# Kernel tuning notes

Hardware: AMD Instinct MI355X
Metric: run time of the kernel (lower is better)

## Reference

```python
import jax, jax.numpy as jnp
import numpy as np

N_ENS = 10   # LSTMs per ensemble
N_OPP = 5    # opponents
H_GEN = 10   # gen LSTM hidden
H_OPP = 5    # opp LSTM hidden


def setup_inputs() -> dict:
    key = jax.random.key(0)
    ks = iter(jax.random.split(key, 32))
    r = lambda shape, s=0.1: jax.random.normal(next(ks), shape, dtype=jnp.float32) * s
    return {
        "x": jax.random.normal(next(ks), (1, 1, 37), dtype=jnp.float32),
        # 10 gen LSTMs (input 12, hidden 10), stacked; torch gate order i,f,g,o
        "W_ih_gen": r((N_ENS, 4 * H_GEN, 12)),
        "W_hh_gen": r((N_ENS, 4 * H_GEN, H_GEN)),
        "b_ih_gen": r((N_ENS, 4 * H_GEN)),
        "b_hh_gen": r((N_ENS, 4 * H_GEN)),
        "h0_gen": r((N_ENS, H_GEN)),
        "c0_gen": r((N_ENS, H_GEN)),
        # 10 opp-game LSTMs (input 4, hidden 5), shared weights across opponents
        "W_ih_game": r((N_ENS, 4 * H_OPP, 4)),
        "W_hh_game": r((N_ENS, 4 * H_OPP, H_OPP)),
        "b_ih_game": r((N_ENS, 4 * H_OPP)),
        "b_hh_game": r((N_ENS, 4 * H_OPP)),
        # per-opponent, per-ensemble-member hidden/cell states
        "h0_game": r((N_OPP, N_ENS, H_OPP)),
        "c0_game": r((N_OPP, N_ENS, H_OPP)),
        # decision MLP
        "W1": r((50, 200)), "b1": r((50,)),
        "W2": r((10, 50)), "b2": r((10,)),
        "W3": r((1, 10)), "b3": r((1,)),
    }


def reference(x, W_ih_gen, W_hh_gen, b_ih_gen, b_hh_gen, h0_gen, c0_gen,
              W_ih_game, W_hh_game, b_ih_game, b_hh_game, h0_game, c0_game,
              W1, b1, W2, b2, W3, b3):
    xv = x[0, 0]  # seq_len = batch = 1 is forced by the 200-feature reshape

    # --- gen ensemble: 10 independent LSTM cells batched as one GEMM ---
    x_gen = xv[:12]
    g = (jnp.einsum('khi,i->kh', W_ih_gen, x_gen)
         + jnp.einsum('khj,kj->kh', W_hh_gen, h0_gen)
         + b_ih_gen + b_hh_gen)                      # [10, 40]
    ig, fg, gg, og = jnp.split(g, 4, axis=-1)
    c_gen = jax.nn.sigmoid(fg) * c0_gen + jax.nn.sigmoid(ig) * jnp.tanh(gg)
    h_gen = jax.nn.sigmoid(og) * jnp.tanh(c_gen)      # [10, 10]
    x_gen_out = h_gen.reshape(-1)                     # [100]

    # --- opponent game ensembles: 5 opps x 10 LSTMs batched ---
    x_opp = xv[12:].reshape(N_OPP, 5)
    active = x_opp[:, 0]
    xin = x_opp[:, 1:]                                # [5, 4]
    g2 = (jnp.einsum('khi,oi->okh', W_ih_game, xin)
          + jnp.einsum('khj,okj->okh', W_hh_game, h0_game)
          + b_ih_game + b_hh_game)                    # [5, 10, 20]
    i2, f2, g2g, o2 = jnp.split(g2, 4, axis=-1)
    c_game = jax.nn.sigmoid(f2) * c0_game + jax.nn.sigmoid(i2) * jnp.tanh(g2g)
    h_game = jax.nn.sigmoid(o2) * jnp.tanh(c_game)    # [5, 10, 5]

    # Source bug preserved: the 'round' loop concatenates x_opp_game (output of
    # the LAST game LSTM, i=9) ten more times; round-LSTM outputs never reach
    # the model output, so they are omitted here.
    feat = jnp.concatenate(
        [h_game.reshape(N_OPP, -1),                     # 10*5 = 50
         jnp.tile(h_game[:, -1, :], (1, N_ENS))],       # 10*5 = 50 (repeated)
        axis=1)                                         # [5, 100]

    # if int(x_active) == 1 -> truncation toward zero then equality with 1
    mask = (jnp.trunc(active) == 1).astype(feat.dtype)  # [5]
    cnt = mask.sum()
    avg = jnp.where(cnt > 0,
                    (mask[:, None] * feat).sum(0) / jnp.maximum(cnt, 1.0),
                    jnp.zeros((100,), feat.dtype))       # [100]

    h1 = jnp.tanh(jnp.concatenate([x_gen_out, avg]) @ W1.T + b1)
    h2 = jnp.tanh(h1 @ W2.T + b2)
    out = jnp.tanh(h2 @ W3.T + b3)
    return out.reshape(1, 1, 1)
```

## Files before the change

### kernel.cpp

```cpp
#include <hip/hip_runtime.h>

__device__ __forceinline__ float sigf(float x) { return 1.0f / (1.0f + expf(-x)); }

__global__ __launch_bounds__(512) void net6max_kernel(
    const float* __restrict__ x,
    const float* __restrict__ W_ih_gen, const float* __restrict__ W_hh_gen,
    const float* __restrict__ b_ih_gen, const float* __restrict__ b_hh_gen,
    const float* __restrict__ h0_gen,  const float* __restrict__ c0_gen,
    const float* __restrict__ W_ih_game, const float* __restrict__ W_hh_game,
    const float* __restrict__ b_ih_game, const float* __restrict__ b_hh_game,
    const float* __restrict__ h0_game, const float* __restrict__ c0_game,
    const float* __restrict__ W1, const float* __restrict__ b1,
    const float* __restrict__ W2, const float* __restrict__ b2,
    const float* __restrict__ W3, const float* __restrict__ b3,
    float* __restrict__ out)
{
    __shared__ float xs[37];
    __shared__ float g_gen[400];
    __shared__ float g2[1000];
    __shared__ float hg[100];
    __shared__ float hgame[250];
    __shared__ float in200[200];
    __shared__ float h1v[50];
    __shared__ float h2v[10];

    const int tid = threadIdx.x;

    if (tid < 37) xs[tid] = x[tid];
    __syncthreads();

    if (tid < 400) {
        const int k = tid / 40, h = tid % 40;
        float s = b_ih_gen[tid] + b_hh_gen[tid];
        const float* wi = W_ih_gen + (k * 40 + h) * 12;
        #pragma unroll
        for (int i = 0; i < 12; ++i) s += wi[i] * xs[i];
        const float* wh = W_hh_gen + (k * 40 + h) * 10;
        const float* h0 = h0_gen + k * 10;
        #pragma unroll
        for (int j = 0; j < 10; ++j) s += wh[j] * h0[j];
        g_gen[tid] = s;
    }
    for (int e = tid; e < 1000; e += 512) {
        const int o = e / 200, rem = e % 200;
        const int k = rem / 20, h = rem % 20;
        float s = b_ih_game[k * 20 + h] + b_hh_game[k * 20 + h];
        const float* wi = W_ih_game + (k * 20 + h) * 4;
        const float* xi = xs + 12 + o * 5 + 1;
        #pragma unroll
        for (int i = 0; i < 4; ++i) s += wi[i] * xi[i];
        const float* wh = W_hh_game + (k * 20 + h) * 5;
        const float* h0 = h0_game + (o * 10 + k) * 5;
        #pragma unroll
        for (int j = 0; j < 5; ++j) s += wh[j] * h0[j];
        g2[e] = s;
    }
    __syncthreads();

    if (tid < 100) {
        const int k = tid / 10, j = tid % 10;
        const float ig = g_gen[k*40 +      j];
        const float fg = g_gen[k*40 + 10 + j];
        const float gg = g_gen[k*40 + 20 + j];
        const float og = g_gen[k*40 + 30 + j];
        const float c  = sigf(fg) * c0_gen[tid] + sigf(ig) * tanhf(gg);
        hg[tid] = sigf(og) * tanhf(c);
    }
    if (tid >= 256 && tid < 506) {
        const int e = tid - 256;
        const int o = e / 50, rem = e % 50, k = rem / 5, j = rem % 5;
        const int base = (o * 10 + k) * 20;
        const float ig = g2[base +      j];
        const float fg = g2[base +  5 + j];
        const float gg = g2[base + 10 + j];
        const float og = g2[base + 15 + j];
        const float c  = sigf(fg) * c0_game[e] + sigf(ig) * tanhf(gg);
        hgame[e] = sigf(og) * tanhf(c);
    }
    __syncthreads();

    if (tid < 100) in200[tid] = hg[tid];
    if (tid >= 128 && tid < 228) {
        const int c = tid - 128;
        float cnt = 0.f, s = 0.f;
        #pragma unroll
        for (int o = 0; o < 5; ++o) {
            const float m = (truncf(xs[12 + o * 5]) == 1.0f) ? 1.0f : 0.0f;
            cnt += m;
            const float f = (c < 50) ? hgame[o * 50 + c]
                                     : hgame[o * 50 + 45 + (c - 50) % 5];
            s += m * f;
        }
        in200[100 + c] = (cnt > 0.f) ? (s / cnt) : 0.f;
    }
    __syncthreads();

    if (tid < 200) {
        const int row = tid >> 2, seg = tid & 3;
        const float* w = W1 + row * 200 + seg * 50;
        const float* v = in200 + seg * 50;
        float p = 0.f;
        #pragma unroll
        for (int c = 0; c < 50; ++c) p += w[c] * v[c];
        p += __shfl_down(p, 2);
        p += __shfl_down(p, 1);
        if (seg == 0) h1v[row] = tanhf(p + b1[row]);
    }
    __syncthreads();

    if (tid < 10) {
        const float* w = W2 + tid * 50;
        float s = b2[tid];
        #pragma unroll
        for (int c = 0; c < 50; ++c) s += w[c] * h1v[c];
        h2v[tid] = tanhf(s);
    }
    __syncthreads();

    if (tid == 0) {
        float s = b3[0];
        #pragma unroll
        for (int c = 0; c < 10; ++c) s += W3[c] * h2v[c];
        out[0] = tanhf(s);
    }
}

extern "C" void kernel_launch(void* const* d_in, const int* in_sizes, int n_in,
                              void* d_out, int out_size, void* d_ws, size_t ws_size,
                              hipStream_t stream) {
    (void)in_sizes; (void)n_in; (void)out_size; (void)d_ws; (void)ws_size;
    net6max_kernel<<<1, 512, 0, stream>>>(
        (const float*)d_in[0],
        (const float*)d_in[1],
        (const float*)d_in[2],
        (const float*)d_in[3],
        (const float*)d_in[4],
        (const float*)d_in[5],
        (const float*)d_in[6],
        (const float*)d_in[7],
        (const float*)d_in[8],
        (const float*)d_in[9],
        (const float*)d_in[10],
        (const float*)d_in[11],
        (const float*)d_in[12],
        (const float*)d_in[13],
        (const float*)d_in[14],
        (const float*)d_in[15],
        (const float*)d_in[16],
        (const float*)d_in[17],
        (const float*)d_in[18],
        (float*)d_out);
}
```

Baseline: 11.63 us.

## Prefetch MLP weights into registers and fuse LSTM gate phases to cut barriers

Each thread now computes all four gates of its LSTM unit and applies the cell update directly, which removes the gate-preactivation shared buffers and one barrier. The W1/W2/W3 weights and biases are loaded into registers at kernel start so their global latency overlaps the LSTM phase. The layer-2 and layer-3 stages are merged into one wavefront using a shuffle reduction, removing another barrier. The block also shrinks to 384 threads. The cost is more registers per thread (two 50-float arrays), which risks spilling, and less parallelism in the gate computation.

Measured after the change: 12.19 us. 4.8% more time.

```diff
diff --git a/kernel.cpp b/kernel.cpp
--- a/kernel.cpp
+++ b/kernel.cpp
@@ -2,7 +2,7 @@
 
 __device__ __forceinline__ float sigf(float x) { return 1.0f / (1.0f + expf(-x)); }
 
-__global__ __launch_bounds__(512) void net6max_kernel(
+__global__ __launch_bounds__(384) void net6max_kernel(
     const float* __restrict__ x,
     const float* __restrict__ W_ih_gen, const float* __restrict__ W_hh_gen,
     const float* __restrict__ b_ih_gen, const float* __restrict__ b_hh_gen,
@@ -15,113 +15,115 @@
     const float* __restrict__ W3, const float* __restrict__ b3,
     float* __restrict__ out)
 {
-    __shared__ float xs[37];
-    __shared__ float g_gen[400];
-    __shared__ float g2[1000];
     __shared__ float hg[100];
     __shared__ float hgame[250];
-    __shared__ float in200[200];
-    __shared__ float h1v[50];
-    __shared__ float h2v[10];
+    __shared__ float avg_s[100];
+    __shared__ float h1v[52];
 
     const int tid = threadIdx.x;
 
-    if (tid < 37) xs[tid] = x[tid];
-    __syncthreads();
+    float w1r[50];
+    float b1r = 0.f;
+    if (tid < 200) {
+        const int row = tid >> 2, seg = tid & 3;
+        const float* w = W1 + row * 200 + seg * 50;
+        #pragma unroll
+        for (int c = 0; c < 50; ++c) w1r[c] = w[c];
+        if (seg == 0) b1r = b1[row];
+    }
+    float w2r[50];
+    float b2r = 0.f, w3r = 0.f, b3r = 0.f;
+    if (tid < 10) {
+        const float* w = W2 + tid * 50;
+        #pragma unroll
+        for (int c = 0; c < 50; ++c) w2r[c] = w[c];
+        b2r = b2[tid];
+        w3r = W3[tid];
+    }
+    if (tid == 0) b3r = b3[0];
 
-    if (tid < 400) {
-        const int k = tid / 40, h = tid % 40;
-        float s = b_ih_gen[tid] + b_hh_gen[tid];
-        const float* wi = W_ih_gen + (k * 40 + h) * 12;
+    if (tid < 100) {
+        const int k = tid / 10, j = tid % 10;
+        float acc[4];
         #pragma unroll
-        for (int i = 0; i < 12; ++i) s += wi[i] * xs[i];
-        const float* wh = W_hh_gen + (k * 40 + h) * 10;
-        const float* h0 = h0_gen + k * 10;
+        for (int g = 0; g < 4; ++g) {
+            const int r = k * 40 + g * 10 + j;
+            float s = b_ih_gen[r] + b_hh_gen[r];
+            const float* wi = W_ih_gen + r * 12;
+            #pragma unroll
+            for (int i = 0; i < 12; ++i) s += wi[i] * x[i];
+            const float* wh = W_hh_gen + r * 10;
+            const float* h0 = h0_gen + k * 10;
+            #pragma unroll
+            for (int jj = 0; jj < 10; ++jj) s += wh[jj] * h0[jj];
+            acc[g] = s;
+        }
+        const float c = sigf(acc[1]) * c0_gen[tid] + sigf(acc[0]) * tanhf(acc[2]);
+        hg[tid] = sigf(acc[3]) * tanhf(c);
+    }
+    if (tid >= 128 && tid < 378) {
+        const int e = tid - 128;
+        const int o = e / 50, rem = e % 50, k = rem / 5, j = rem % 5;
+        float acc[4];
         #pragma unroll
-        for (int j = 0; j < 10; ++j) s += wh[j] * h0[j];
-        g_gen[tid] = s;
-    }
-    for (int e = tid; e < 1000; e += 512) {
-        const int o = e / 200, rem = e % 200;
-        const int k = rem / 20, h = rem % 20;
-        float s = b_ih_game[k * 20 + h] + b_hh_game[k * 20 + h];
-        const float* wi = W_ih_game + (k * 20 + h) * 4;
-        const float* xi = xs + 12 + o * 5 + 1;
-        #pragma unroll
-        for (int i = 0; i < 4; ++i) s += wi[i] * xi[i];
-        const float* wh = W_hh_game + (k * 20 + h) * 5;
-        const float* h0 = h0_game + (o * 10 + k) * 5;
-        #pragma unroll
-        for (int j = 0; j < 5; ++j) s += wh[j] * h0[j];
-        g2[e] = s;
+        for (int g = 0; g < 4; ++g) {
+            const int r = k * 20 + g * 5 + j;
+            float s = b_ih_game[r] + b_hh_game[r];
+            const float* wi = W_ih_game + r * 4;
+            const float* xi = x + 12 + o * 5 + 1;
+            #pragma unroll
+            for (int i = 0; i < 4; ++i) s += wi[i] * xi[i];
+            const float* wh = W_hh_game + r * 5;
+            const float* h0 = h0_game + (o * 10 + k) * 5;
+            #pragma unroll
+            for (int jj = 0; jj < 5; ++jj) s += wh[jj] * h0[jj];
+            acc[g] = s;
+        }
+        const float c = sigf(acc[1]) * c0_game[e] + sigf(acc[0]) * tanhf(acc[2]);
+        hgame[e] = sigf(acc[3]) * tanhf(c);
     }
     __syncthreads();
 
     if (tid < 100) {
-        const int k = tid / 10, j = tid % 10;
-        const float ig = g_gen[k*40 +      j];
-        const float fg = g_gen[k*40 + 10 + j];
-        const float gg = g_gen[k*40 + 20 + j];
-        const float og = g_gen[k*40 + 30 + j];
-        const float c  = sigf(fg) * c0_gen[tid] + sigf(ig) * tanhf(gg);
-        hg[tid] = sigf(og) * tanhf(c);
-    }
-    if (tid >= 256 && tid < 506) {
-        const int e = tid - 256;
-        const int o = e / 50, rem = e % 50, k = rem / 5, j = rem % 5;
-        const int base = (o * 10 + k) * 20;
-        const float ig = g2[base +      j];
-        const float fg = g2[base +  5 + j];
-        const float gg = g2[base + 10 + j];
-        const float og = g2[base + 15 + j];
-        const float c  = sigf(fg) * c0_game[e] + sigf(ig) * tanhf(gg);
-        hgame[e] = sigf(og) * tanhf(c);
-    }
-    __syncthreads();
-
-    if (tid < 100) in200[tid] = hg[tid];
-    if (tid >= 128 && tid < 228) {
-        const int c = tid - 128;
         float cnt = 0.f, s = 0.f;
         #pragma unroll
         for (int o = 0; o < 5; ++o) {
-            const float m = (truncf(xs[12 + o * 5]) == 1.0f) ? 1.0f : 0.0f;
+            const float m = (truncf(x[12 + o * 5]) == 1.0f) ? 1.0f : 0.0f;
             cnt += m;
-            const float f = (c < 50) ? hgame[o * 50 + c]
-                                     : hgame[o * 50 + 45 + (c - 50) % 5];
+            const float f = (tid < 50) ? hgame[o * 50 + tid]
+                                       : hgame[o * 50 + 45 + (tid - 50) % 5];
             s += m * f;
         }
-        in200[100 + c] = (cnt > 0.f) ? (s / cnt) : 0.f;
+        avg_s[tid] = (cnt > 0.f) ? (s / cnt) : 0.f;
     }
     __syncthreads();
 
     if (tid < 200) {
         const int row = tid >> 2, seg = tid & 3;
-        const float* w = W1 + row * 200 + seg * 50;
-        const float* v = in200 + seg * 50;
+        const float* v = (seg < 2) ? (hg + seg * 50) : (avg_s + (seg - 2) * 50);
         float p = 0.f;
         #pragma unroll
-        for (int c = 0; c < 50; ++c) p += w[c] * v[c];
+        for (int c = 0; c < 50; ++c) p += w1r[c] * v[c];
         p += __shfl_down(p, 2);
         p += __shfl_down(p, 1);
-        if (seg == 0) h1v[row] = tanhf(p + b1[row]);
+        if (seg == 0) h1v[row] = tanhf(p + b1r);
     }
     __syncthreads();
 
-    if (tid < 10) {
-        const float* w = W2 + tid * 50;
-        float s = b2[tid];
-        #pragma unroll
-        for (int c = 0; c < 50; ++c) s += w[c] * h1v[c];
-        h2v[tid] = tanhf(s);
-    }
-    __syncthreads();
-
-    if (tid == 0) {
-        float s = b3[0];
-        #pragma unroll
-        for (int c = 0; c < 10; ++c) s += W3[c] * h2v[c];
-        out[0] = tanhf(s);
+    if (tid < 64) {
+        float h2 = 0.f;
+        if (tid < 10) {
+            float s = b2r;
+            #pragma unroll
+            for (int c = 0; c < 50; ++c) s += w2r[c] * h1v[c];
+            h2 = tanhf(s);
+        }
+        float p = (tid < 10) ? w3r * h2 : 0.f;
+        p += __shfl_xor(p, 8);
+        p += __shfl_xor(p, 4);
+        p += __shfl_xor(p, 2);
+        p += __shfl_xor(p, 1);
+        if (tid == 0) out[0] = tanhf(p + b3r);
     }
 }
 
@@ -129,7 +131,7 @@
                               void* d_out, int out_size, void* d_ws, size_t ws_size,
                               hipStream_t stream) {
     (void)in_sizes; (void)n_in; (void)out_size; (void)d_ws; (void)ws_size;
-    net6max_kernel<<<1, 512, 0, stream>>>(
+    net6max_kernel<<<1, 384, 0, stream>>>(
         (const float*)d_in[0],
         (const float*)d_in[1],
         (const float*)d_in[2],
```
